# Optimization experiments

Measured on AMD Instinct MI355X. Metric: run time of the kernel, lower is better.

Reference implementation:

```python
import jax, jax.numpy as jnp
import numpy as np

# PEPS grid configuration (matches init_kwargs)
X, Y = 4, 4            # xnodes, ynodes
D = 6                  # bond_dim
P = 2                  # features_in (physical dim)
F = 10                 # features_out (forced by result.view([10]))
CX, CY = X // 2, Y // 2  # center node carries the output leg
BATCH = 2048


def node_labels(i, j):
    # bond labels after the physical index is contracted away; axis order: up, left, down, right, out
    labs = []
    if i > 0: labs.append(f'v{i-1}_{j}')   # up bond (shared with row i-1)
    if j > 0: labs.append(f'h{i}_{j-1}')   # left bond (shared with col j-1)
    if i < X - 1: labs.append(f'v{i}_{j}') # down bond
    if j < Y - 1: labs.append(f'h{i}_{j}') # right bond
    if (i, j) == (CX, CY): labs.append('o')  # output leg on center node
    return labs


def node_shape(i, j):
    shp = [P]  # physical axis first (input_nodes[i][j][0] ^ peps_nodes[i][j][0])
    shp += [D] * (int(i > 0) + int(j > 0) + int(i < X - 1) + int(j < Y - 1))
    if (i, j) == (CX, CY): shp.append(F)
    return tuple(shp)


def setup_inputs() -> dict:
    key = jax.random.key(0)
    keys = jax.random.split(key, X * Y + 1)
    inp = {"x": jax.random.normal(keys[0], (BATCH, X, Y, P), dtype=jnp.float32)}
    k = 1
    for i in range(X):
        for j in range(Y):
            # simple_peps uniform init with std=0.01
            inp[f"w{i}{j}"] = jax.random.uniform(keys[k], node_shape(i, j), dtype=jnp.float32, minval=-0.01, maxval=0.01)
            k += 1
    return inp


def _td(a, alabs, b, blabs):
    """Label-tracked tensordot over all shared bond labels."""
    shared = [l for l in alabs if l in blabs]
    ai = [alabs.index(l) for l in shared]
    bi = [blabs.index(l) for l in shared]
    out = jnp.tensordot(a, b, axes=(ai, bi))
    labs = [l for l in alabs if l not in shared] + [l for l in blabs if l not in shared]
    return out, labs


def _contract_sample(xs, ws):
    # xs: [X, Y, P] one sample; ws: list-of-lists of node tensors
    # 1) contract each input vector into its PEPS node over the physical axis,
    #    then L2-normalize each contracted node (as in func())
    nodes = []
    for i in range(X):
        row = []
        for j in range(Y):
            t = jnp.tensordot(xs[i, j], ws[i][j], axes=(0, 0))
            t = t / jnp.linalg.norm(t)
            row.append(t)
        nodes.append(row)
    # 2) exact contraction of the 2D network, row-by-row boundary sweep
    cur, labs = nodes[0][0], node_labels(0, 0)
    for j in range(1, Y):
        cur, labs = _td(cur, labs, nodes[0][j], node_labels(0, j))
    for i in range(1, X):
        for j in range(Y):
            cur, labs = _td(cur, labs, nodes[i][j], node_labels(i, j))
    out = cur.reshape(F)  # result.view([10])
    return out / jnp.linalg.norm(out)


def reference(x, w00, w01, w02, w03, w10, w11, w12, w13,
              w20, w21, w22, w23, w30, w31, w32, w33):
    ws = [[w00, w01, w02, w03],
          [w10, w11, w12, w13],
          [w20, w21, w22, w23],
          [w30, w31, w32, w33]]
    return jax.vmap(lambda s: _contract_sample(s, ws))(x)  # [B, F]
```

## Files before the change

kernel.cpp:

```cpp
#include <hip/hip_runtime.h>
#include <math.h>

#define NTHREADS 256

struct PW {
    const float* w[16];
    int perp[16];
};

__global__ __launch_bounds__(NTHREADS) void gram16(PW pw, float* __restrict__ g) {
    const int n = blockIdx.x;
    const float* __restrict__ W = pw.w[n];
    const int m = pw.perp[n];
    float s00 = 0.f, s01 = 0.f, s11 = 0.f;
    for (int e = threadIdx.x; e < m; e += NTHREADS) {
        float a = W[e], b = W[m + e];
        s00 += a * a; s01 += a * b; s11 += b * b;
    }
    for (int off = 32; off > 0; off >>= 1) {
        s00 += __shfl_down(s00, off, 64);
        s01 += __shfl_down(s01, off, 64);
        s11 += __shfl_down(s11, off, 64);
    }
    __shared__ float red[4][3];
    const int lane = threadIdx.x & 63, wv = threadIdx.x >> 6;
    if (lane == 0) { red[wv][0] = s00; red[wv][1] = s01; red[wv][2] = s11; }
    __syncthreads();
    if (threadIdx.x == 0) {
        float t0 = 0.f, t1 = 0.f, t2 = 0.f;
        for (int i = 0; i < 4; i++) { t0 += red[i][0]; t1 += red[i][1]; t2 += red[i][2]; }
        g[n * 3 + 0] = t0; g[n * 3 + 1] = t1; g[n * 3 + 2] = t2;
    }
}

constexpr int C1 = 0, C2 = 1296, C3 = 2592, PB = 3888;
constexpr int T00 = 4104, T01 = 4140, T10 = 4356, T11 = 4572;
constexpr int T02 = 5868, T03 = 6084, T13 = 6120, T12 = 6336;
constexpr int T30 = 7632, T20 = 7668, T31 = 7884, T21 = 8100;
constexpr int T23 = 9396, T33 = 9612, T32 = 9648;
constexpr int ARENA = 9864;

template<int M, int DST>
__device__ __forceinline__ void tmat2(float* __restrict__ lds, const float* __restrict__ W,
                                      float a0, float b0, float a1, float b1, int tid) {
    for (int e = tid; e < 2 * M; e += NTHREADS) {
        const int s = (e >= M) ? 1 : 0;
        const int idx = e - s * M;
        const float al = s ? a1 : a0;
        const float be = s ? b1 : b0;
        lds[s * ARENA + DST + idx] = al * W[idx] + be * W[M + idx];
    }
}

template<int X1, int X2, int Y1, int Y2, int U, int L, int TX,
         int AX1, int AX2, int AU, int AL,
         int BU, int BLS, int BY1, int BY2,
         int OX1, int OX2, int OY1, int OY2,
         int AOFF, int BOFF, int OOFF>
__device__ __forceinline__ void step2(float* __restrict__ lds, int tid) {
    constexpr int XB = X2 / TX;
    constexpr int TILES = X1 * XB * Y1;
    constexpr int TOT = 2 * TILES;
    for (int t = tid; t < TOT; t += NTHREADS) {
        const int sl = t / TILES;
        const int r = t - sl * TILES;
        const int x1 = r / (XB * Y1);
        const int rm = r - x1 * (XB * Y1);
        const int xb = rm / Y1;
        const int y1 = rm - xb * Y1;
        const float* __restrict__ Ab = lds + sl * ARENA + AOFF + x1 * AX1 + xb * TX * AX2;
        const float* __restrict__ Bb = lds + sl * ARENA + BOFF + y1 * BY1;
        float acc[TX][Y2];
#pragma unroll
        for (int i = 0; i < TX; i++)
#pragma unroll
            for (int t2 = 0; t2 < Y2; t2++) acc[i][t2] = 0.f;
#pragma unroll
        for (int u = 0; u < U; u++) {
#pragma unroll
            for (int l = 0; l < L; l++) {
                float a[TX];
#pragma unroll
                for (int i = 0; i < TX; i++) a[i] = Ab[i * AX2 + u * AU + l * AL];
                const float* __restrict__ Bp = Bb + u * BU + l * BLS;
#pragma unroll
                for (int t2 = 0; t2 < Y2; t2++) {
                    const float bv = Bp[t2 * BY2];
#pragma unroll
                    for (int i = 0; i < TX; i++) acc[i][t2] += a[i] * bv;
                }
            }
        }
        float* __restrict__ Ob = lds + sl * ARENA + OOFF + x1 * OX1 + xb * TX * OX2 + y1 * OY1;
#pragma unroll
        for (int i = 0; i < TX; i++)
#pragma unroll
            for (int t2 = 0; t2 < Y2; t2++) Ob[i * OX2 + t2 * OY2] = acc[i][t2];
    }
}

__global__ __launch_bounds__(NTHREADS) void peps_main(const float* __restrict__ x, PW pw,
                                                      const float* __restrict__ gram,
                                                      float* __restrict__ out) {
    __shared__ float lds[2 * ARENA];
    __shared__ float cfa[2][16], cfb[2][16];
    __shared__ float red[4][2][10];

    const int tid = threadIdx.x;
    const int s0 = blockIdx.x * 2;

    if (tid < 32) {
        const int sl = tid >> 4, n = tid & 15;
        const float a = x[(s0 + sl) * 32 + n * 2 + 0];
        const float b = x[(s0 + sl) * 32 + n * 2 + 1];
        const float g0 = gram[n * 3 + 0], g1 = gram[n * 3 + 1], g2 = gram[n * 3 + 2];
        const float inv = 1.f / sqrtf(a * a * g0 + 2.f * a * b * g1 + b * b * g2);
        cfa[sl][n] = a * inv; cfb[sl][n] = b * inv;
    }
    __syncthreads();

#define TM(M, DST, WI) tmat2<M, DST>(lds, pw.w[WI], cfa[0][WI], cfb[0][WI], cfa[1][WI], cfb[1][WI], tid)
    TM(36, T00, 0);  TM(216, T01, 1);  TM(216, T10, 4);  TM(1296, T11, 5);
    TM(216, T02, 2); TM(36, T03, 3);   TM(216, T13, 7);  TM(1296, T12, 6);
    TM(36, T30, 12); TM(216, T20, 8);  TM(216, T31, 13); TM(1296, T21, 9);
    TM(216, T23, 11); TM(36, T33, 15); TM(216, T32, 14);
#undef TM
    __syncthreads();

#define SYNC __syncthreads()
    step2<1, 6, 6, 6, 6, 1, 2,  0, 6, 1, 0,   36, 0, 6, 1,   0, 36, 6, 1,  T00, T01, PB>(lds, tid); SYNC;
    step2<1, 36, 6, 6, 6, 1, 2,  0, 1, 36, 0,  36, 0, 6, 1,   0, 36, 6, 1,  PB, T10, C1>(lds, tid); SYNC;
    step2<6, 6, 6, 6, 6, 6, 2,  36, 6, 216, 1, 216, 36, 6, 1, 216, 36, 6, 1, C1, T11, C2>(lds, tid); SYNC;
    step2<1, 36, 1, 6, 6, 1, 2,  0, 6, 1, 0,   6, 0, 0, 1,    0, 6, 0, 1,   T02, T03, PB>(lds, tid); SYNC;
    step2<1, 36, 6, 6, 6, 1, 2,  0, 6, 1, 0,   36, 0, 6, 1,   0, 36, 6, 1,  PB, T13, C1>(lds, tid); SYNC;
    step2<6, 6, 6, 6, 6, 6, 2,  36, 6, 216, 1, 36, 6, 216, 1, 216, 36, 6, 1, T12, C1, C3>(lds, tid); SYNC;
    step2<6, 6, 6, 6, 6, 6, 2,  36, 6, 216, 1, 6, 216, 36, 1, 216, 36, 6, 1, C2, C3, C1>(lds, tid); SYNC;
    step2<1, 6, 6, 6, 6, 1, 2,  0, 1, 6, 0,    6, 0, 36, 1,   0, 36, 6, 1,  T30, T20, PB>(lds, tid); SYNC;
    step2<1, 36, 6, 6, 6, 1, 2,  0, 1, 36, 0,  6, 0, 36, 1,   0, 36, 6, 1,  PB, T31, C2>(lds, tid); SYNC;
    step2<6, 6, 6, 6, 6, 6, 2,  216, 1, 36, 6, 36, 6, 216, 1, 216, 36, 6, 1, C2, T21, C3>(lds, tid); SYNC;
    step2<6, 6, 6, 6, 6, 6, 2,  6, 1, 216, 36, 216, 6, 36, 1, 216, 36, 6, 1, C1, C3, C2>(lds, tid); SYNC;
    step2<6, 6, 1, 6, 6, 1, 2,  36, 6, 1, 0,   6, 0, 0, 1,    36, 6, 0, 1,  T23, T33, PB>(lds, tid); SYNC;
    step2<6, 6, 6, 6, 6, 1, 2,  36, 6, 1, 0,   1, 0, 36, 6,   216, 1, 6, 36, PB, T32, C1>(lds, tid); SYNC;
    step2<6, 6, 6, 6, 6, 6, 2,  216, 1, 36, 6, 216, 36, 6, 1, 216, 36, 6, 1, C2, C1, C3>(lds, tid); SYNC;

    {
        const float a0 = cfa[0][10], b0 = cfb[0][10];
        const float a1 = cfa[1][10], b1 = cfb[1][10];
        const float* __restrict__ w0 = pw.w[10];
        const float* __restrict__ w1 = w0 + 12960;
        float p0[10], p1[10];
#pragma unroll
        for (int o = 0; o < 10; o++) { p0[o] = 0.f; p1[o] = 0.f; }
        for (int e = tid; e < 1296; e += NTHREADS) {
            const float E0 = lds[C3 + e];
            const float E1 = lds[ARENA + C3 + e];
            const float* __restrict__ q0 = w0 + e * 10;
            const float* __restrict__ q1 = w1 + e * 10;
#pragma unroll
            for (int o = 0; o < 10; o++) {
                const float v0 = q0[o], v1 = q1[o];
                p0[o] += E0 * (a0 * v0 + b0 * v1);
                p1[o] += E1 * (a1 * v0 + b1 * v1);
            }
        }
#pragma unroll
        for (int o = 0; o < 10; o++)
            for (int off = 32; off > 0; off >>= 1) {
                p0[o] += __shfl_down(p0[o], off, 64);
                p1[o] += __shfl_down(p1[o], off, 64);
            }
        const int lane = tid & 63, wv = tid >> 6;
        if (lane == 0) {
#pragma unroll
            for (int o = 0; o < 10; o++) { red[wv][0][o] = p0[o]; red[wv][1][o] = p1[o]; }
        }
        __syncthreads();
        if (tid < 2) {
            float r[10];
            float ss = 0.f;
#pragma unroll
            for (int o = 0; o < 10; o++) {
                r[o] = red[0][tid][o] + red[1][tid][o] + red[2][tid][o] + red[3][tid][o];
                ss += r[o] * r[o];
            }
            const float inv = 1.f / sqrtf(ss);
#pragma unroll
            for (int o = 0; o < 10; o++) out[(s0 + tid) * 10 + o] = r[o] * inv;
        }
    }
#undef SYNC
}

extern "C" void kernel_launch(void* const* d_in, const int* in_sizes, int n_in,
                              void* d_out, int out_size, void* d_ws, size_t ws_size,
                              hipStream_t stream) {
    PW pw;
    for (int k = 0; k < 16; k++) {
        pw.w[k] = (const float*)d_in[1 + k];
        pw.perp[k] = in_sizes[1 + k] / 2;
    }
    float* gram = (float*)d_ws;
    gram16<<<16, NTHREADS, 0, stream>>>(pw, gram);

    const float* x = (const float*)d_in[0];
    const int B = out_size / 10;
    peps_main<<<B / 2, NTHREADS, 0, stream>>>(x, pw, gram, (float*)d_out);
}
```

Before: 157.8 us.

## Process one sample per 128-thread block with interleaved node loads and smaller LDS arena

The main kernel now handles one sample per block with 128 threads instead of two samples with 256 threads. Contracted node tensors are built just in time, interleaved with the contraction steps, and written into a small set of reused scratch buffers, which shrinks LDS from about 79KB to about 23KB per block. The aim is higher occupancy and overlap of global weight loads with LDS matmul work. In exchange the grid doubles, each block reads the weights once per sample instead of once per pair, and some barriers are merged, which could expose races if buffer reuse is wrong.

```diff
diff --git a/kernel.cpp b/kernel.cpp
--- a/kernel.cpp
+++ b/kernel.cpp
@@ -1,19 +1,17 @@
 #include <hip/hip_runtime.h>
 #include <math.h>
 
-#define NTHREADS 256
+#define NT 128
+#define NTG 256
 
-struct PW {
-    const float* w[16];
-    int perp[16];
-};
+struct PW { const float* w[16]; int perp[16]; };
 
-__global__ __launch_bounds__(NTHREADS) void gram16(PW pw, float* __restrict__ g) {
+__global__ __launch_bounds__(NTG) void gram16(PW pw, float* __restrict__ g) {
     const int n = blockIdx.x;
     const float* __restrict__ W = pw.w[n];
     const int m = pw.perp[n];
     float s00 = 0.f, s01 = 0.f, s11 = 0.f;
-    for (int e = threadIdx.x; e < m; e += NTHREADS) {
+    for (int e = threadIdx.x; e < m; e += NTG) {
         float a = W[e], b = W[m + e];
         s00 += a * a; s01 += a * b; s11 += b * b;
     }
@@ -33,23 +31,14 @@
     }
 }
 
-constexpr int C1 = 0, C2 = 1296, C3 = 2592, PB = 3888;
-constexpr int T00 = 4104, T01 = 4140, T10 = 4356, T11 = 4572;
-constexpr int T02 = 5868, T03 = 6084, T13 = 6120, T12 = 6336;
-constexpr int T30 = 7632, T20 = 7668, T31 = 7884, T21 = 8100;
-constexpr int T23 = 9396, T33 = 9612, T32 = 9648;
-constexpr int ARENA = 9864;
+constexpr int BA = 0, BB = 1296, BC = 2592, BD = 3888;
+constexpr int PBo = 5184, SA = 5400, SB = 5616, SC = 5832;
+constexpr int ASZ = 5868;
 
 template<int M, int DST>
-__device__ __forceinline__ void tmat2(float* __restrict__ lds, const float* __restrict__ W,
-                                      float a0, float b0, float a1, float b1, int tid) {
-    for (int e = tid; e < 2 * M; e += NTHREADS) {
-        const int s = (e >= M) ? 1 : 0;
-        const int idx = e - s * M;
-        const float al = s ? a1 : a0;
-        const float be = s ? b1 : b0;
-        lds[s * ARENA + DST + idx] = al * W[idx] + be * W[M + idx];
-    }
+__device__ __forceinline__ void tmat(float* __restrict__ lds, const float* __restrict__ W,
+                                     float al, float be, int tid) {
+    for (int e = tid; e < M; e += NT) lds[DST + e] = al * W[e] + be * W[M + e];
 }
 
 template<int X1, int X2, int Y1, int Y2, int U, int L, int TX,
@@ -57,19 +46,16 @@
          int BU, int BLS, int BY1, int BY2,
          int OX1, int OX2, int OY1, int OY2,
          int AOFF, int BOFF, int OOFF>
-__device__ __forceinline__ void step2(float* __restrict__ lds, int tid) {
+__device__ __forceinline__ void step(float* __restrict__ lds, int tid) {
     constexpr int XB = X2 / TX;
     constexpr int TILES = X1 * XB * Y1;
-    constexpr int TOT = 2 * TILES;
-    for (int t = tid; t < TOT; t += NTHREADS) {
-        const int sl = t / TILES;
-        const int r = t - sl * TILES;
+    for (int r = tid; r < TILES; r += NT) {
         const int x1 = r / (XB * Y1);
         const int rm = r - x1 * (XB * Y1);
         const int xb = rm / Y1;
         const int y1 = rm - xb * Y1;
-        const float* __restrict__ Ab = lds + sl * ARENA + AOFF + x1 * AX1 + xb * TX * AX2;
-        const float* __restrict__ Bb = lds + sl * ARENA + BOFF + y1 * BY1;
+        const float* __restrict__ Ab = lds + AOFF + x1 * AX1 + xb * TX * AX2;
+        const float* __restrict__ Bb = lds + BOFF + y1 * BY1;
         float acc[TX][Y2];
 #pragma unroll
         for (int i = 0; i < TX; i++)
@@ -91,7 +77,7 @@
                 }
             }
         }
-        float* __restrict__ Ob = lds + sl * ARENA + OOFF + x1 * OX1 + xb * TX * OX2 + y1 * OY1;
+        float* __restrict__ Ob = lds + OOFF + x1 * OX1 + xb * TX * OX2 + y1 * OY1;
 #pragma unroll
         for (int i = 0; i < TX; i++)
 #pragma unroll
@@ -99,96 +85,95 @@
     }
 }
 
-__global__ __launch_bounds__(NTHREADS) void peps_main(const float* __restrict__ x, PW pw,
-                                                      const float* __restrict__ gram,
-                                                      float* __restrict__ out) {
-    __shared__ float lds[2 * ARENA];
-    __shared__ float cfa[2][16], cfb[2][16];
-    __shared__ float red[4][2][10];
+__global__ __launch_bounds__(NT) void peps_main(const float* __restrict__ x, PW pw,
+                                                const float* __restrict__ gram,
+                                                float* __restrict__ out) {
+    __shared__ float lds[ASZ];
+    __shared__ float cfa[16], cfb[16];
+    __shared__ float red[2][10];
 
     const int tid = threadIdx.x;
-    const int s0 = blockIdx.x * 2;
+    const int s = blockIdx.x;
 
-    if (tid < 32) {
-        const int sl = tid >> 4, n = tid & 15;
-        const float a = x[(s0 + sl) * 32 + n * 2 + 0];
-        const float b = x[(s0 + sl) * 32 + n * 2 + 1];
-        const float g0 = gram[n * 3 + 0], g1 = gram[n * 3 + 1], g2 = gram[n * 3 + 2];
+    if (tid < 16) {
+        const float a = x[s * 32 + tid * 2 + 0];
+        const float b = x[s * 32 + tid * 2 + 1];
+        const float g0 = gram[tid * 3 + 0], g1 = gram[tid * 3 + 1], g2 = gram[tid * 3 + 2];
         const float inv = 1.f / sqrtf(a * a * g0 + 2.f * a * b * g1 + b * b * g2);
-        cfa[sl][n] = a * inv; cfb[sl][n] = b * inv;
+        cfa[tid] = a * inv; cfb[tid] = b * inv;
     }
     __syncthreads();
 
-#define TM(M, DST, WI) tmat2<M, DST>(lds, pw.w[WI], cfa[0][WI], cfb[0][WI], cfa[1][WI], cfb[1][WI], tid)
-    TM(36, T00, 0);  TM(216, T01, 1);  TM(216, T10, 4);  TM(1296, T11, 5);
-    TM(216, T02, 2); TM(36, T03, 3);   TM(216, T13, 7);  TM(1296, T12, 6);
-    TM(36, T30, 12); TM(216, T20, 8);  TM(216, T31, 13); TM(1296, T21, 9);
-    TM(216, T23, 11); TM(36, T33, 15); TM(216, T32, 14);
+#define TM(M, DST, WI) tmat<M, DST>(lds, pw.w[WI], cfa[WI], cfb[WI], tid)
+#define SYNC __syncthreads()
+
+    TM(36, SC, 0); TM(216, SA, 1); SYNC;
+    step<1, 6, 6, 6, 6, 1, 1,  0, 6, 1, 0,   36, 0, 6, 1,   0, 36, 6, 1,  SC, SA, PBo>(lds, tid);
+    TM(216, SB, 4); SYNC;
+    step<1, 36, 6, 6, 6, 1, 2,  0, 1, 36, 0,  36, 0, 6, 1,   0, 36, 6, 1,  PBo, SB, BA>(lds, tid);
+    TM(1296, BB, 5); SYNC;
+    step<6, 6, 6, 6, 6, 6, 2,  36, 6, 216, 1, 216, 36, 6, 1, 216, 36, 6, 1, BA, BB, BC>(lds, tid);
+    TM(216, SA, 2); TM(36, SC, 3); SYNC;
+    step<1, 36, 1, 6, 6, 1, 1,  0, 6, 1, 0,   6, 0, 0, 1,    0, 6, 0, 1,   SA, SC, PBo>(lds, tid);
+    TM(216, SB, 7); SYNC;
+    step<1, 36, 6, 6, 6, 1, 2,  0, 6, 1, 0,   36, 0, 6, 1,   0, 36, 6, 1,  PBo, SB, BA>(lds, tid);
+    TM(1296, BB, 6); SYNC;
+    step<6, 6, 6, 6, 6, 6, 2,  36, 6, 216, 1, 36, 6, 216, 1, 216, 36, 6, 1, BB, BA, BD>(lds, tid);
+    TM(36, SC, 12); TM(216, SA, 8); SYNC;
+    step<6, 6, 6, 6, 6, 6, 2,  36, 6, 216, 1, 6, 216, 36, 1, 216, 36, 6, 1, BC, BD, BA>(lds, tid);
+    step<1, 6, 6, 6, 6, 1, 1,  0, 1, 6, 0,    6, 0, 36, 1,   0, 36, 6, 1,  SC, SA, PBo>(lds, tid);
+    TM(216, SB, 13); SYNC;
+    step<1, 36, 6, 6, 6, 1, 2,  0, 1, 36, 0,  6, 0, 36, 1,   0, 36, 6, 1,  PBo, SB, BC>(lds, tid);
+    TM(1296, BD, 9); SYNC;
+    step<6, 6, 6, 6, 6, 6, 2,  216, 1, 36, 6, 36, 6, 216, 1, 216, 36, 6, 1, BC, BD, BB>(lds, tid);
+    TM(216, SA, 11); TM(36, SC, 15); SYNC;
+    step<6, 6, 6, 6, 6, 6, 2,  6, 1, 216, 36, 216, 6, 36, 1, 216, 36, 6, 1, BA, BB, BC>(lds, tid);
+    step<6, 6, 1, 6, 6, 1, 1,  36, 6, 1, 0,   6, 0, 0, 1,    36, 6, 0, 1,  SA, SC, PBo>(lds, tid);
+    TM(216, SB, 14); SYNC;
+    step<6, 6, 6, 6, 6, 1, 2,  36, 6, 1, 0,   1, 0, 36, 6,   216, 1, 6, 36, PBo, SB, BA>(lds, tid);
+    SYNC;
+    step<6, 6, 6, 6, 6, 6, 2,  216, 1, 36, 6, 216, 36, 6, 1, 216, 36, 6, 1, BC, BA, BB>(lds, tid);
+    SYNC;
 #undef TM
-    __syncthreads();
-
-#define SYNC __syncthreads()
-    step2<1, 6, 6, 6, 6, 1, 2,  0, 6, 1, 0,   36, 0, 6, 1,   0, 36, 6, 1,  T00, T01, PB>(lds, tid); SYNC;
-    step2<1, 36, 6, 6, 6, 1, 2,  0, 1, 36, 0,  36, 0, 6, 1,   0, 36, 6, 1,  PB, T10, C1>(lds, tid); SYNC;
-    step2<6, 6, 6, 6, 6, 6, 2,  36, 6, 216, 1, 216, 36, 6, 1, 216, 36, 6, 1, C1, T11, C2>(lds, tid); SYNC;
-    step2<1, 36, 1, 6, 6, 1, 2,  0, 6, 1, 0,   6, 0, 0, 1,    0, 6, 0, 1,   T02, T03, PB>(lds, tid); SYNC;
-    step2<1, 36, 6, 6, 6, 1, 2,  0, 6, 1, 0,   36, 0, 6, 1,   0, 36, 6, 1,  PB, T13, C1>(lds, tid); SYNC;
-    step2<6, 6, 6, 6, 6, 6, 2,  36, 6, 216, 1, 36, 6, 216, 1, 216, 36, 6, 1, T12, C1, C3>(lds, tid); SYNC;
-    step2<6, 6, 6, 6, 6, 6, 2,  36, 6, 216, 1, 6, 216, 36, 1, 216, 36, 6, 1, C2, C3, C1>(lds, tid); SYNC;
-    step2<1, 6, 6, 6, 6, 1, 2,  0, 1, 6, 0,    6, 0, 36, 1,   0, 36, 6, 1,  T30, T20, PB>(lds, tid); SYNC;
-    step2<1, 36, 6, 6, 6, 1, 2,  0, 1, 36, 0,  6, 0, 36, 1,   0, 36, 6, 1,  PB, T31, C2>(lds, tid); SYNC;
-    step2<6, 6, 6, 6, 6, 6, 2,  216, 1, 36, 6, 36, 6, 216, 1, 216, 36, 6, 1, C2, T21, C3>(lds, tid); SYNC;
-    step2<6, 6, 6, 6, 6, 6, 2,  6, 1, 216, 36, 216, 6, 36, 1, 216, 36, 6, 1, C1, C3, C2>(lds, tid); SYNC;
-    step2<6, 6, 1, 6, 6, 1, 2,  36, 6, 1, 0,   6, 0, 0, 1,    36, 6, 0, 1,  T23, T33, PB>(lds, tid); SYNC;
-    step2<6, 6, 6, 6, 6, 1, 2,  36, 6, 1, 0,   1, 0, 36, 6,   216, 1, 6, 36, PB, T32, C1>(lds, tid); SYNC;
-    step2<6, 6, 6, 6, 6, 6, 2,  216, 1, 36, 6, 216, 36, 6, 1, 216, 36, 6, 1, C2, C1, C3>(lds, tid); SYNC;
+#undef SYNC
 
     {
-        const float a0 = cfa[0][10], b0 = cfb[0][10];
-        const float a1 = cfa[1][10], b1 = cfb[1][10];
+        const float al = cfa[10], be = cfb[10];
         const float* __restrict__ w0 = pw.w[10];
         const float* __restrict__ w1 = w0 + 12960;
-        float p0[10], p1[10];
+        float p[10];
 #pragma unroll
-        for (int o = 0; o < 10; o++) { p0[o] = 0.f; p1[o] = 0.f; }
-        for (int e = tid; e < 1296; e += NTHREADS) {
-            const float E0 = lds[C3 + e];
-            const float E1 = lds[ARENA + C3 + e];
+        for (int o = 0; o < 10; o++) p[o] = 0.f;
+        for (int e = tid; e < 1296; e += NT) {
+            const float Ev = lds[BB + e];
             const float* __restrict__ q0 = w0 + e * 10;
             const float* __restrict__ q1 = w1 + e * 10;
 #pragma unroll
-            for (int o = 0; o < 10; o++) {
-                const float v0 = q0[o], v1 = q1[o];
-                p0[o] += E0 * (a0 * v0 + b0 * v1);
-                p1[o] += E1 * (a1 * v0 + b1 * v1);
-            }
+            for (int o = 0; o < 10; o++) p[o] += Ev * (al * q0[o] + be * q1[o]);
         }
 #pragma unroll
         for (int o = 0; o < 10; o++)
-            for (int off = 32; off > 0; off >>= 1) {
-                p0[o] += __shfl_down(p0[o], off, 64);
-                p1[o] += __shfl_down(p1[o], off, 64);
-            }
+            for (int off = 32; off > 0; off >>= 1)
+                p[o] += __shfl_down(p[o], off, 64);
         const int lane = tid & 63, wv = tid >> 6;
         if (lane == 0) {
 #pragma unroll
-            for (int o = 0; o < 10; o++) { red[wv][0][o] = p0[o]; red[wv][1][o] = p1[o]; }
+            for (int o = 0; o < 10; o++) red[wv][o] = p[o];
         }
         __syncthreads();
-        if (tid < 2) {
+        if (tid == 0) {
             float r[10];
             float ss = 0.f;
 #pragma unroll
             for (int o = 0; o < 10; o++) {
-                r[o] = red[0][tid][o] + red[1][tid][o] + red[2][tid][o] + red[3][tid][o];
+                r[o] = red[0][o] + red[1][o];
                 ss += r[o] * r[o];
             }
             const float inv = 1.f / sqrtf(ss);
 #pragma unroll
-            for (int o = 0; o < 10; o++) out[(s0 + tid) * 10 + o] = r[o] * inv;
+            for (int o = 0; o < 10; o++) out[s * 10 + o] = r[o] * inv;
         }
     }
-#undef SYNC
 }
 
 extern "C" void kernel_launch(void* const* d_in, const int* in_sizes, int n_in,
@@ -200,9 +185,9 @@
         pw.perp[k] = in_sizes[1 + k] / 2;
     }
     float* gram = (float*)d_ws;
-    gram16<<<16, NTHREADS, 0, stream>>>(pw, gram);
+    gram16<<<16, NTG, 0, stream>>>(pw, gram);
 
     const float* x = (const float*)d_in[0];
     const int B = out_size / 10;
-    peps_main<<<B / 2, NTHREADS, 0, stream>>>(x, pw, gram, (float*)d_out);
+    peps_main<<<B, NT, 0, stream>>>(x, pw, gram, (float*)d_out);
 }
```

Measured after the change: 159.4 us. About the same (+1.0%).
